# Performance work log

Measured on AMD Instinct MI355X. Metric: run time of the kernel, lower is better.

The kernel has to match this reference:

```python
import jax, jax.numpy as jnp
import numpy as np

D_MODEL = 1024
N_HEADS = 16
D_HEAD = D_MODEL // N_HEADS
HIDDEN = 4 * D_MODEL
EPS = 1e-5
ROPE_BASE = 10000.0


def layernorm(x, g, b):
    mu = jnp.mean(x, axis=-1, keepdims=True)
    var = jnp.mean((x - mu) ** 2, axis=-1, keepdims=True)
    return (x - mu) * jax.lax.rsqrt(var + EPS) * g + b


def rope(t, pos):
    # t: (B, N, D), pos: (N,) int -> rotary transform over D (half-split pairs)
    half = t.shape[-1] // 2
    inv_freq = 1.0 / (ROPE_BASE ** (jnp.arange(half, dtype=jnp.float32) / half))
    ang = pos.astype(jnp.float32)[:, None] * inv_freq  # (N, half)
    cos, sin = jnp.cos(ang), jnp.sin(ang)
    t1, t2 = t[..., :half], t[..., half:]
    return jnp.concatenate([t1 * cos - t2 * sin, t1 * sin + t2 * cos], axis=-1)


def setup_inputs() -> dict:
    key = jax.random.key(0)
    ks = jax.random.split(key, 12)
    B, N, D, H = 2, 2048, D_MODEL, HIDDEN
    s = 0.02
    return {
        "x": jax.random.normal(ks[0], (B, N, D), jnp.float32),
        "pos": jnp.arange(N, dtype=jnp.int32),
        "Wq": jax.random.normal(ks[1], (D, D), jnp.float32) * s,
        "bq": jnp.zeros((D,), jnp.float32),
        "Wk": jax.random.normal(ks[2], (D, D), jnp.float32) * s,
        "bk": jnp.zeros((D,), jnp.float32),
        "Wv": jax.random.normal(ks[3], (D, D), jnp.float32) * s,
        "bv": jnp.zeros((D,), jnp.float32),
        "Wo": jax.random.normal(ks[4], (D, D), jnp.float32) * s,
        "bo": jnp.zeros((D,), jnp.float32),
        "g1": jnp.ones((D,), jnp.float32),
        "b1": jnp.zeros((D,), jnp.float32),
        "g2": jnp.ones((D,), jnp.float32),
        "b2": jnp.zeros((D,), jnp.float32),
        "W1": jax.random.normal(ks[5], (D, H), jnp.float32) * s,
        "bm1": jnp.zeros((H,), jnp.float32),
        "W2": jax.random.normal(ks[6], (H, D), jnp.float32) * s,
        "bm2": jnp.zeros((D,), jnp.float32),
    }


def reference(x, pos, Wq, bq, Wk, bk, Wv, bv, Wo, bo, g1, b1, g2, b2, W1, bm1, W2, bm2):
    B, N, D = x.shape
    Hh, dh = N_HEADS, D_HEAD

    # --- attention sublayer (pre-norm) ---
    h = layernorm(x, g1, b1)
    q = h @ Wq + bq
    k = h @ Wk + bk
    v = h @ Wv + bv
    q = rope(q, pos)
    k = rope(k, pos)
    # split heads: (B, Hh, N, dh)
    q = q.reshape(B, N, Hh, dh).transpose(0, 2, 1, 3)
    k = k.reshape(B, N, Hh, dh).transpose(0, 2, 1, 3)
    v = v.reshape(B, N, Hh, dh).transpose(0, 2, 1, 3)
    scores = jnp.einsum("bhqd,bhkd->bhqk", q, k) / jnp.sqrt(jnp.float32(dh))
    attn = jax.nn.softmax(scores, axis=-1)
    ctx = jnp.einsum("bhqk,bhkd->bhqd", attn, v)
    ctx = ctx.transpose(0, 2, 1, 3).reshape(B, N, D)
    x = x + ctx @ Wo + bo

    # --- MLP sublayer (pre-norm, exact GELU) ---
    h = layernorm(x, g2, b2)
    h = jax.nn.gelu(h @ W1 + bm1, approximate=False)
    x = x + h @ W2 + bm2
    return x
```

## Files before the change

kernel.cpp:

```cpp
#include <hip/hip_runtime.h>

typedef __bf16 bf16x8 __attribute__((ext_vector_type(8)));
typedef __bf16 bf16x4 __attribute__((ext_vector_type(4)));
typedef float  f32x4  __attribute__((ext_vector_type(4)));

#define D_MODEL 1024
#define SEQ     2048
#define BATCH   2
#define NH      16
#define DH      64
#define HID     4096
#define ROWS    (BATCH*SEQ)

static __device__ __forceinline__ void gl_lds16(const __bf16* g, __bf16* l) {
  __builtin_amdgcn_global_load_lds(
      (const __attribute__((address_space(1))) unsigned int*)g,
      (__attribute__((address_space(3))) unsigned int*)l, 16, 0, 0);
}

__global__ __launch_bounds__(256) void ln_kernel(
    const float* __restrict__ x, const float* __restrict__ g,
    const float* __restrict__ b, __bf16* __restrict__ out)
{
  int row = blockIdx.x;
  const float* xr = x + (size_t)row * D_MODEL;
  int i0 = threadIdx.x * 4;
  f32x4 xv = *(const f32x4*)(xr + i0);
  float s  = xv[0] + xv[1] + xv[2] + xv[3];
  float ss = xv[0]*xv[0] + xv[1]*xv[1] + xv[2]*xv[2] + xv[3]*xv[3];
#pragma unroll
  for (int off = 1; off < 64; off <<= 1) {
    s  += __shfl_xor(s,  off, 64);
    ss += __shfl_xor(ss, off, 64);
  }
  __shared__ float red[8];
  int wave = threadIdx.x >> 6;
  if ((threadIdx.x & 63) == 0) { red[wave] = s; red[4 + wave] = ss; }
  __syncthreads();
  s  = red[0] + red[1] + red[2] + red[3];
  ss = red[4] + red[5] + red[6] + red[7];
  float mu  = s * (1.0f / D_MODEL);
  float var = ss * (1.0f / D_MODEL) - mu * mu;
  float inv = rsqrtf(var + 1e-5f);
  f32x4 gv = *(const f32x4*)(g + i0);
  f32x4 bv = *(const f32x4*)(b + i0);
  bf16x4 ov;
#pragma unroll
  for (int j = 0; j < 4; ++j)
    ov[j] = (__bf16)((xv[j] - mu) * inv * gv[j] + bv[j]);
  *(bf16x4*)(out + (size_t)row * D_MODEL + i0) = ov;
}

__global__ __launch_bounds__(256) void convT_kernel(
    const float* __restrict__ W, __bf16* __restrict__ Wt, int K, int N)
{
  __shared__ float T[32][33];
  int n0 = blockIdx.x * 32, k0 = blockIdx.y * 32;
  int r  = threadIdx.x >> 3;
  int c4 = (threadIdx.x & 7) * 4;
  f32x4 v = *(const f32x4*)(W + (size_t)(k0 + r) * N + n0 + c4);
#pragma unroll
  for (int i = 0; i < 4; ++i) T[r][c4 + i] = v[i];
  __syncthreads();
  bf16x4 o;
#pragma unroll
  for (int i = 0; i < 4; ++i) o[i] = (__bf16)T[c4 + i][r];
  *(bf16x4*)(Wt + (size_t)(n0 + r) * K + k0 + c4) = o;
}

__global__ void biascat_kernel(const float* __restrict__ a,
                               const float* __restrict__ b,
                               const float* __restrict__ c,
                               float* __restrict__ o)
{
  int i = blockIdx.x * 256 + threadIdx.x;
  o[i] = i < 1024 ? a[i] : (i < 2048 ? b[i - 1024] : c[i - 2048]);
}

__global__ __launch_bounds__(512, 2) void gemm256(
    const __bf16* __restrict__ A, const __bf16* __restrict__ Bt,
    const float* __restrict__ bias, const float* __restrict__ resid,
    void* __restrict__ Cv, int M, int N, int K, int act, int c_fp32)
{
  __shared__ __bf16 As[2][256 * 64];
  __shared__ __bf16 Bs[2][256 * 64];
  int tid = threadIdx.x, lane = tid & 63, wv = tid >> 6;
  int quad = lane >> 4, l16 = lane & 15;
  int wr = wv >> 2, wc = wv & 3;
  int gx = M >> 8, gy = N >> 8;
  int nwg = gx * gy;
  int xcd = blockIdx.x & 7;
  int q = nwg >> 3, r8 = nwg & 7;
  int wg = (xcd < r8 ? xcd * (q + 1) : r8 * (q + 1) + (xcd - r8) * q) + (blockIdx.x >> 3);
  int row0 = (wg % gx) << 8;
  int col0 = (wg / gx) << 8;
  int s_r  = lane >> 3;
  int s_src = ((lane & 7) ^ s_r) * 8;
  int sw = l16 & 7;
  int NT = K >> 6;
  f32x4 acc[8][4] = {};

#define G256_STAGE(kt, b)                                                     \
  {                                                                           \
    int k0_ = (kt) * 64;                                                      \
    _Pragma("unroll")                                                         \
    for (int rd = 0; rd < 4; ++rd) {                                          \
      int rrow = rd * 64 + wv * 8 + s_r;                                      \
      gl_lds16(A  + (size_t)(row0 + rrow) * K + k0_ + s_src,                  \
               &As[b][rd * 4096 + wv * 512]);                                 \
      gl_lds16(Bt + (size_t)(col0 + rrow) * K + k0_ + s_src,                  \
               &Bs[b][rd * 4096 + wv * 512]);                                 \
    }                                                                         \
  }

  G256_STAGE(0, 0);
  G256_STAGE(1, 1);

  for (int t = 0; t < NT; ++t) {
    if (t + 1 < NT) asm volatile("s_waitcnt vmcnt(8)" ::: "memory");
    else            asm volatile("s_waitcnt vmcnt(0)" ::: "memory");
    __builtin_amdgcn_s_barrier();
    const __bf16* Ab = &As[t & 1][0];
    const __bf16* Bb = &Bs[t & 1][0];
    __builtin_amdgcn_s_setprio(1);
#pragma unroll
    for (int kk = 0; kk < 2; ++kk) {
      int slot = ((kk * 4 + quad) ^ sw) * 8;
      bf16x8 bfr[4];
#pragma unroll
      for (int j = 0; j < 4; ++j)
        bfr[j] = *(const bf16x8*)(Bb + (wc * 64 + j * 16 + l16) * 64 + slot);
      bf16x8 afr[8];
#pragma unroll
      for (int i = 0; i < 8; ++i)
        afr[i] = *(const bf16x8*)(Ab + (wr * 128 + i * 16 + l16) * 64 + slot);
#pragma unroll
      for (int i = 0; i < 8; ++i)
#pragma unroll
        for (int j = 0; j < 4; ++j)
          acc[i][j] = __builtin_amdgcn_mfma_f32_16x16x32_bf16(afr[i], bfr[j], acc[i][j], 0, 0, 0);
    }
    __builtin_amdgcn_s_setprio(0);
    __builtin_amdgcn_s_barrier();
    if (t + 2 < NT) G256_STAGE(t + 2, t & 1);
  }

#pragma unroll
  for (int i = 0; i < 8; ++i) {
    int grow = row0 + wr * 128 + i * 16 + quad * 4;
#pragma unroll
    for (int j = 0; j < 4; ++j) {
      int gcol = col0 + wc * 64 + j * 16 + l16;
      float bsv = bias[gcol];
#pragma unroll
      for (int r = 0; r < 4; ++r) {
        size_t off = (size_t)(grow + r) * N + gcol;
        float v = acc[i][j][r] + bsv;
        if (act) v = 0.5f * v * (1.0f + erff(v * 0.70710678118654752f));
        if (resid) v += resid[off];
        if (c_fp32) ((float*)Cv)[off] = v;
        else        ((__bf16*)Cv)[off] = (__bf16)v;
      }
    }
  }
}

__global__ __launch_bounds__(256) void gemm128(
    const __bf16* __restrict__ A, const __bf16* __restrict__ Bt,
    const float* __restrict__ bias, const float* __restrict__ resid,
    void* __restrict__ Cv, int M, int N, int K, int act, int c_fp32)
{
  __shared__ __bf16 As[128 * 64];
  __shared__ __bf16 Bs[128 * 64];
  int tid = threadIdx.x, lane = tid & 63, wv = tid >> 6;
  int quad = lane >> 4, l16 = lane & 15;
  int wr = wv >> 1, wc = wv & 1;
  int gx = M >> 7, gy = N >> 7;
  int blk = blockIdx.x;
  int xcd = blk & 7, t = blk >> 3;
  int row0 = (t % gx) * 128;
  int col0 = (xcd * (gy >> 3) + t / gx) * 128;
  int s_r8 = lane >> 3;
  int s_c8 = lane & 7;
  int s_src = (s_c8 ^ s_r8) * 8;
  int sw = l16 & 7;
  f32x4 acc[4][4] = {};

  for (int k0 = 0; k0 < K; k0 += 64) {
#pragma unroll
    for (int p = 0; p < 4; ++p) {
      int r = p * 32 + wv * 8 + s_r8;
      gl_lds16(A  + (size_t)(row0 + r) * K + k0 + s_src, As + p * 2048 + wv * 512);
      gl_lds16(Bt + (size_t)(col0 + r) * K + k0 + s_src, Bs + p * 2048 + wv * 512);
    }
    __syncthreads();
#pragma unroll
    for (int kk = 0; kk < 2; ++kk) {
      int slot = ((kk * 4 + quad) ^ sw) * 8;
      bf16x8 af[4], bf[4];
#pragma unroll
      for (int i = 0; i < 4; ++i) {
        af[i] = *(const bf16x8*)(As + (wr * 64 + i * 16 + l16) * 64 + slot);
        bf[i] = *(const bf16x8*)(Bs + (wc * 64 + i * 16 + l16) * 64 + slot);
      }
#pragma unroll
      for (int i = 0; i < 4; ++i)
#pragma unroll
        for (int j = 0; j < 4; ++j)
          acc[i][j] = __builtin_amdgcn_mfma_f32_16x16x32_bf16(af[i], bf[j], acc[i][j], 0, 0, 0);
    }
    __syncthreads();
  }
#pragma unroll
  for (int i = 0; i < 4; ++i) {
    int grow = row0 + wr * 64 + i * 16 + quad * 4;
#pragma unroll
    for (int j = 0; j < 4; ++j) {
      int gcol = col0 + wc * 64 + j * 16 + l16;
      float bsv = bias[gcol];
#pragma unroll
      for (int r = 0; r < 4; ++r) {
        size_t off = (size_t)(grow + r) * N + gcol;
        float v = acc[i][j][r] + bsv;
        if (act) v = 0.5f * v * (1.0f + erff(v * 0.70710678118654752f));
        if (resid) v += resid[off];
        if (c_fp32) ((float*)Cv)[off] = v;
        else        ((__bf16*)Cv)[off] = (__bf16)v;
      }
    }
  }
}

__global__ __launch_bounds__(256) void gemm64x128(
    const __bf16* __restrict__ A, const __bf16* __restrict__ Bt,
    const float* __restrict__ bias, const float* __restrict__ resid,
    void* __restrict__ Cv, int M, int N, int K, int act, int c_fp32)
{
  __shared__ __bf16 As[2][64 * 64];
  __shared__ __bf16 Bs[2][128 * 64];
  int tid = threadIdx.x, lane = tid & 63, wv = tid >> 6;
  int quad = lane >> 4, l16 = lane & 15;
  int wr = wv >> 1, wc = wv & 1;
  int gx = M >> 6, gy = N >> 7;
  int blk = blockIdx.x;
  int xcd = blk & 7, t = blk >> 3;
  int row0 = (t % gx) * 64;
  int col0 = (xcd * (gy >> 3) + t / gx) * 128;
  int s_r8 = lane >> 3;
  int s_c8 = lane & 7;
  int s_src = (s_c8 ^ s_r8) * 8;
  int sw = l16 & 7;
  int NT = K >> 6;
  f32x4 acc[2][4] = {};

#define G64_STAGE(kt, b)                                                      \
  {                                                                           \
    int k0_ = (kt) * 64;                                                      \
    _Pragma("unroll")                                                         \
    for (int p = 0; p < 4; ++p) {                                             \
      int r = p * 32 + wv * 8 + s_r8;                                         \
      if (p < 2)                                                              \
        gl_lds16(A + (size_t)(row0 + r) * K + k0_ + s_src,                    \
                 &As[b][p * 2048 + wv * 512]);                                \
      gl_lds16(Bt + (size_t)(col0 + r) * K + k0_ + s_src,                     \
               &Bs[b][p * 2048 + wv * 512]);                                  \
    }                                                                         \
  }

  G64_STAGE(0, 0);
  G64_STAGE(1, 1);

  for (int tt = 0; tt < NT; ++tt) {
    if (tt + 1 < NT) asm volatile("s_waitcnt vmcnt(6)" ::: "memory");
    else             asm volatile("s_waitcnt vmcnt(0)" ::: "memory");
    __builtin_amdgcn_s_barrier();
    const __bf16* Ab = &As[tt & 1][0];
    const __bf16* Bb = &Bs[tt & 1][0];
    __builtin_amdgcn_s_setprio(1);
#pragma unroll
    for (int kk = 0; kk < 2; ++kk) {
      int slot = ((kk * 4 + quad) ^ sw) * 8;
      bf16x8 af[2], bf[4];
#pragma unroll
      for (int i = 0; i < 2; ++i)
        af[i] = *(const bf16x8*)(Ab + (wr * 32 + i * 16 + l16) * 64 + slot);
#pragma unroll
      for (int j = 0; j < 4; ++j)
        bf[j] = *(const bf16x8*)(Bb + (wc * 64 + j * 16 + l16) * 64 + slot);
#pragma unroll
      for (int i = 0; i < 2; ++i)
#pragma unroll
        for (int j = 0; j < 4; ++j)
          acc[i][j] = __builtin_amdgcn_mfma_f32_16x16x32_bf16(af[i], bf[j], acc[i][j], 0, 0, 0);
    }
    __builtin_amdgcn_s_setprio(0);
    __builtin_amdgcn_s_barrier();
    if (tt + 2 < NT) G64_STAGE(tt + 2, tt & 1);
  }

#pragma unroll
  for (int i = 0; i < 2; ++i) {
    int grow = row0 + wr * 32 + i * 16 + quad * 4;
#pragma unroll
    for (int j = 0; j < 4; ++j) {
      int gcol = col0 + wc * 64 + j * 16 + l16;
      float bsv = bias[gcol];
#pragma unroll
      for (int r = 0; r < 4; ++r) {
        size_t off = (size_t)(grow + r) * N + gcol;
        float v = acc[i][j][r] + bsv;
        if (act) v = 0.5f * v * (1.0f + erff(v * 0.70710678118654752f));
        if (resid) v += resid[off];
        if (c_fp32) ((float*)Cv)[off] = v;
        else        ((__bf16*)Cv)[off] = (__bf16)v;
      }
    }
  }
}

__global__ __launch_bounds__(256) void rope_repack(
    const __bf16* __restrict__ qkv, const int* __restrict__ pos,
    __bf16* __restrict__ Qh, __bf16* __restrict__ Kh)
{
  int row = blockIdx.x;
  int b = row >> 11, n = row & (SEQ - 1);
  float p = (float)pos[n];
  const __bf16* qr = qkv + (size_t)row * 3072;
  const float QS = 0.125f * 1.44269504088896f;
#pragma unroll
  for (int t = 0; t < 2; ++t) {
    int i = threadIdx.x + t * 256;
    float fr  = expf(-9.210340371976184f * ((float)i * (1.0f / 512.0f)));
    float ang = p * fr;
    float sn, c;
    sincosf(ang, &sn, &c);
    float q1 = (float)qr[i],        q2 = (float)qr[512 + i];
    float k1 = (float)qr[1024 + i], k2 = (float)qr[1536 + i];
    int h1 = i >> 6, d1 = i & 63;
    int h2 = (i + 512) >> 6;
    size_t o1 = ((size_t)(b * NH + h1) * SEQ + n) * DH + d1;
    size_t o2 = ((size_t)(b * NH + h2) * SEQ + n) * DH + d1;
    Qh[o1] = (__bf16)((q1 * c - q2 * sn) * QS);
    Qh[o2] = (__bf16)((q1 * sn + q2 * c) * QS);
    Kh[o1] = (__bf16)(k1 * c - k2 * sn);
    Kh[o2] = (__bf16)(k1 * sn + k2 * c);
  }
}

__global__ __launch_bounds__(256) void vtrans_kernel(
    const __bf16* __restrict__ Vsrc, int vstride, __bf16* __restrict__ Vt,
    int blocked)
{
  __shared__ __bf16 T[64][72];
  int bh = blockIdx.x;
  int kb = blockIdx.y * 64;
  int b = bh >> 4, h = bh & 15;
  int tid = threadIdx.x;
#pragma unroll
  for (int t = 0; t < 2; ++t) {
    int u = tid + t * 256;
    int r = u >> 3, seg = (u & 7) * 8;
    bf16x8 v = *(const bf16x8*)(Vsrc + (size_t)(b * SEQ + kb + r) * vstride + h * DH + seg);
    *(bf16x8*)(&T[r][seg]) = v;
  }
  __syncthreads();
#pragma unroll
  for (int t = 0; t < 2; ++t) {
    int u = tid + t * 256;
    int d = u >> 3, ks = (u & 7) * 8;
    bf16x8 o;
#pragma unroll
    for (int i = 0; i < 8; ++i) o[i] = T[ks + i][d];
    if (blocked) {
      int key = kb + ks;
      *(bf16x8*)(Vt + (((size_t)bh * (SEQ / 128) + (key >> 7)) * DH + d) * 128 + (key & 127)) = o;
    } else {
      *(bf16x8*)(Vt + ((size_t)bh * DH + d) * SEQ + kb + ks) = o;
    }
  }
}

#define KS 136
__global__ __launch_bounds__(512) void attn_split(
    const __bf16* __restrict__ Qh, const __bf16* __restrict__ Kh,
    const __bf16* __restrict__ Vt, __bf16* __restrict__ pacc,
    float* __restrict__ pml)
{
  __shared__ __bf16 Ks[128 * 64];
  __shared__ __bf16 Vs[64 * 128];
  __shared__ __bf16 Pl[8][16 * KS];
  int tid = threadIdx.x, lane = tid & 63, wave = tid >> 6;
  int quad = lane >> 4, l16 = lane & 15;
  int blk = blockIdx.x;
  int split = blk >> 9;
  int rr = blk & 511;
  int bh  = ((rr & 7) << 2) | ((rr >> 3) & 3);
  int q128 = rr >> 5;
  int q0 = q128 * 128 + wave * 16;
  const __bf16* qbase = Qh + (size_t)bh * SEQ * DH;
  const __bf16* kbase = Kh + (size_t)bh * SEQ * DH;
  const __bf16* vbase = Vt + (size_t)bh * SEQ * DH;
  const __bf16* qp = qbase + (size_t)(q0 + l16) * DH + quad * 8;
  bf16x8 qf0 = *(const bf16x8*)(qp);
  bf16x8 qf1 = *(const bf16x8*)(qp + 32);
  float lrow[4] = {0.f, 0.f, 0.f, 0.f};
  f32x4 acc[4] = {};
  __bf16* pw = &Pl[wave][0];
  int s_kr = lane >> 3;
  int s_k8 = lane & 7;
  int s_vd = lane >> 4;
  int s_vs = lane & 15;
  int sw8  = l16 & 7;

  int kb0 = split * (SEQ / 2);
  for (int it = 0; it < (SEQ / 2) / 128; ++it) {
    int kb = kb0 + it * 128;
    const __bf16* kt = kbase + (size_t)kb * DH;
    const __bf16* vt = vbase + (size_t)(kb >> 7) * (DH * 128);
    __syncthreads();
#pragma unroll
    for (int p = 0; p < 2; ++p) {
      int key0 = p * 64 + wave * 8;
      int swz  = (key0 >> 3) & 7;
      gl_lds16(kt + (key0 + s_kr) * DH + ((s_k8 ^ swz) * 8), Ks + p * 4096 + wave * 512);
      int d = p * 32 + wave * 4 + s_vd;
      gl_lds16(vt + d * 128 + ((s_vs ^ (d & 15)) * 8), Vs + p * 4096 + wave * 512);
    }
    __syncthreads();
    f32x4 s[8];
#pragma unroll
    for (int j = 0; j < 8; ++j) {
      const __bf16* kr = Ks + (l16 * 8 + j) * 64;
      bf16x8 kf0 = *(const bf16x8*)(kr + (quad ^ sw8) * 8);
      bf16x8 kf1 = *(const bf16x8*)(kr + ((quad ^ sw8) ^ 4) * 8);
      f32x4 z = {};
      z = __builtin_amdgcn_mfma_f32_16x16x32_bf16(qf0, kf0, z, 0, 0, 0);
      s[j] = __builtin_amdgcn_mfma_f32_16x16x32_bf16(qf1, kf1, z, 0, 0, 0);
    }
#pragma unroll
    for (int r = 0; r < 4; ++r) {
      bf16x8 pv;
      float rs = 0.f;
#pragma unroll
      for (int j = 0; j < 8; ++j) {
        float pj = exp2f(s[j][r]);
        rs += pj;
        pv[j] = (__bf16)pj;
      }
      lrow[r] += rs;
      *(bf16x8*)(pw + (quad * 4 + r) * KS + l16 * 8) = pv;
    }
#pragma unroll
    for (int kk = 0; kk < 4; ++kk) {
      bf16x8 pf = *(const bf16x8*)(pw + l16 * KS + kk * 32 + quad * 8);
#pragma unroll
      for (int j = 0; j < 4; ++j) {
        int d = j * 16 + l16;
        bf16x8 vf = *(const bf16x8*)(Vs + d * 128 + (((kk * 4 + quad) ^ (d & 15)) * 8));
        acc[j] = __builtin_amdgcn_mfma_f32_16x16x32_bf16(pf, vf, acc[j], 0, 0, 0);
      }
    }
  }
#pragma unroll
  for (int r = 0; r < 4; ++r)
#pragma unroll
    for (int off = 1; off < 16; off <<= 1) lrow[r] += __shfl_xor(lrow[r], off, 64);
#pragma unroll
  for (int r = 0; r < 4; ++r) {
    int brow = wave * 16 + quad * 4 + r;
#pragma unroll
    for (int j = 0; j < 4; ++j)
      pacc[((size_t)blk * 128 + brow) * 64 + j * 16 + l16] = (__bf16)acc[j][r];
    if (l16 == 0) {
      pml[(size_t)blk * 256 + brow]       = 0.f;
      pml[(size_t)blk * 256 + 128 + brow] = lrow[r];
    }
  }
}

__global__ __launch_bounds__(256) void attn_combine(
    const __bf16* __restrict__ pacc, const float* __restrict__ pml,
    __bf16* __restrict__ ctx)
{
  int bq = blockIdx.x;
  int q64 = bq & 31, bh = bq >> 5;
  int b = bh >> 4, h = bh & 15;
  int q128 = q64 >> 1, half = q64 & 1;
  int tid = threadIdx.x;
  int r = tid >> 2;
  int c = (tid & 3) * 16;
  int brow = half * 64 + r;
  int blk0 = q128 * 32 + (bh & 3) * 8 + (bh >> 2);
  int blk1 = blk0 + 512;
  float m0 = pml[(size_t)blk0 * 256 + brow], l0 = pml[(size_t)blk0 * 256 + 128 + brow];
  float m1 = pml[(size_t)blk1 * 256 + brow], l1 = pml[(size_t)blk1 * 256 + 128 + brow];
  float m = fmaxf(m0, m1);
  float w0 = __expf(m0 - m), w1 = __expf(m1 - m);
  float inv = 1.0f / (w0 * l0 + w1 * l1);
  size_t r0 = ((size_t)blk0 * 128 + brow) * 64 + c;
  size_t r1 = ((size_t)blk1 * 128 + brow) * 64 + c;
  size_t ob = ((size_t)(b * SEQ) + q64 * 64 + r) * D_MODEL + h * DH + c;
#pragma unroll
  for (int g = 0; g < 2; ++g) {
    bf16x8 a0 = *(const bf16x8*)(pacc + r0 + g * 8);
    bf16x8 a1 = *(const bf16x8*)(pacc + r1 + g * 8);
    bf16x8 o;
#pragma unroll
    for (int i = 0; i < 8; ++i)
      o[i] = (__bf16)((w0 * (float)a0[i] + w1 * (float)a1[i]) * inv);
    *(bf16x8*)(ctx + ob + g * 8) = o;
  }
}

__global__ __launch_bounds__(256) void rope_inplace(
    __bf16* __restrict__ ql, __bf16* __restrict__ kl,
    const int* __restrict__ pos, int stride)
{
  int row = blockIdx.x;
  int n = row & (SEQ - 1);
  float p = (float)pos[n];
  const size_t rbase = (size_t)row * stride;
#pragma unroll
  for (int t = 0; t < 2; ++t) {
    int i = threadIdx.x + t * 256;
    float fr  = expf(-9.210340371976184f * ((float)i * (1.0f / 512.0f)));
    float ang = p * fr;
    float sn, c;
    sincosf(ang, &sn, &c);
    float q1 = (float)ql[rbase + i], q2 = (float)ql[rbase + 512 + i];
    float k1 = (float)kl[rbase + i], k2 = (float)kl[rbase + 512 + i];
    ql[rbase + i]       = (__bf16)(q1 * c - q2 * sn);
    ql[rbase + 512 + i] = (__bf16)(q1 * sn + q2 * c);
    kl[rbase + i]       = (__bf16)(k1 * c - k2 * sn);
    kl[rbase + 512 + i] = (__bf16)(k1 * sn + k2 * c);
  }
}

__global__ __launch_bounds__(256) void attn_kernel(
    const __bf16* __restrict__ Q, const __bf16* __restrict__ K,
    const __bf16* __restrict__ Vt, __bf16* __restrict__ ctx, int qkstride)
{
  __shared__ __bf16 Pl[4][16 * KS];
  int tid = threadIdx.x, lane = tid & 63, wave = tid >> 6;
  int quad = lane >> 4, l16 = lane & 15;
  int blk = blockIdx.x;
  int q64 = blk & 31;
  int bh  = blk >> 5;
  int b = bh >> 4, h = bh & 15;
  int q0 = q64 * 64 + wave * 16;
  const __bf16* qbase = Q + (size_t)b * SEQ * qkstride + h * DH;
  const __bf16* kbase = K + (size_t)b * SEQ * qkstride + h * DH;
  const __bf16* vbase = Vt + (size_t)bh * DH * SEQ;
  const __bf16* qp = qbase + (size_t)(q0 + l16) * qkstride + quad * 8;
  bf16x8 qf0 = *(const bf16x8*)(qp);
  bf16x8 qf1 = *(const bf16x8*)(qp + 32);
  float mrow[4] = {-1e30f, -1e30f, -1e30f, -1e30f};
  float lrow[4] = {0.f, 0.f, 0.f, 0.f};
  f32x4 acc[4] = {};
  __bf16* pw = &Pl[wave][0];

  for (int kb = 0; kb < SEQ; kb += 128) {
    f32x4 s[8];
#pragma unroll
    for (int j = 0; j < 8; ++j) {
      const __bf16* kp = kbase + (size_t)(kb + l16 * 8 + j) * qkstride + quad * 8;
      bf16x8 kf0 = *(const bf16x8*)(kp);
      bf16x8 kf1 = *(const bf16x8*)(kp + 32);
      f32x4 z = {};
      z = __builtin_amdgcn_mfma_f32_16x16x32_bf16(qf0, kf0, z, 0, 0, 0);
      z = __builtin_amdgcn_mfma_f32_16x16x32_bf16(qf1, kf1, z, 0, 0, 0);
#pragma unroll
      for (int r = 0; r < 4; ++r) s[j][r] = z[r] * 0.125f;
    }
#pragma unroll
    for (int r = 0; r < 4; ++r) {
      float mx = s[0][r];
#pragma unroll
      for (int j = 1; j < 8; ++j) mx = fmaxf(mx, s[j][r]);
#pragma unroll
      for (int off = 1; off < 16; off <<= 1) mx = fmaxf(mx, __shfl_xor(mx, off, 64));
      float mn = fmaxf(mrow[r], mx);
      float al = __expf(mrow[r] - mn);
      float p[8], rs = 0.f;
#pragma unroll
      for (int j = 0; j < 8; ++j) { p[j] = __expf(s[j][r] - mn); rs += p[j]; }
#pragma unroll
      for (int off = 1; off < 16; off <<= 1) rs += __shfl_xor(rs, off, 64);
      lrow[r] = lrow[r] * al + rs;
      mrow[r] = mn;
#pragma unroll
      for (int j = 0; j < 4; ++j) acc[j][r] *= al;
      bf16x8 pv;
#pragma unroll
      for (int j = 0; j < 8; ++j) pv[j] = (__bf16)p[j];
      *(bf16x8*)(pw + (quad * 4 + r) * KS + l16 * 8) = pv;
    }
#pragma unroll
    for (int kk = 0; kk < 4; ++kk) {
      bf16x8 pf = *(const bf16x8*)(pw + l16 * KS + kk * 32 + quad * 8);
#pragma unroll
      for (int j = 0; j < 4; ++j) {
        bf16x8 vf = *(const bf16x8*)(vbase + (size_t)(j * 16 + l16) * SEQ + kb + kk * 32 + quad * 8);
        acc[j] = __builtin_amdgcn_mfma_f32_16x16x32_bf16(pf, vf, acc[j], 0, 0, 0);
      }
    }
  }
#pragma unroll
  for (int r = 0; r < 4; ++r) {
    int row = q0 + quad * 4 + r;
    float inv = 1.0f / lrow[r];
    size_t obase = ((size_t)(b * SEQ) + row) * D_MODEL + h * DH;
#pragma unroll
    for (int j = 0; j < 4; ++j)
      ctx[obase + j * 16 + l16] = (__bf16)(acc[j][r] * inv);
  }
}

extern "C" void kernel_launch(void* const* d_in, const int* in_sizes, int n_in,
                              void* d_out, int out_size, void* d_ws, size_t ws_size,
                              hipStream_t stream)
{
  const float* x   = (const float*)d_in[0];
  const int*   pos = (const int*)  d_in[1];
  const float* Wq  = (const float*)d_in[2];
  const float* bq  = (const float*)d_in[3];
  const float* Wk  = (const float*)d_in[4];
  const float* bk  = (const float*)d_in[5];
  const float* Wv  = (const float*)d_in[6];
  const float* bv  = (const float*)d_in[7];
  const float* Wo  = (const float*)d_in[8];
  const float* bo  = (const float*)d_in[9];
  const float* g1  = (const float*)d_in[10];
  const float* b1  = (const float*)d_in[11];
  const float* g2  = (const float*)d_in[12];
  const float* b2  = (const float*)d_in[13];
  const float* W1  = (const float*)d_in[14];
  const float* bm1 = (const float*)d_in[15];
  const float* W2  = (const float*)d_in[16];
  const float* bm2 = (const float*)d_in[17];
  float* out = (float*)d_out;

  const size_t MB = 1024 * 1024;
  char* w = (char*)d_ws;
  dim3 blk(256);
  dim3 blk512(512);
  dim3 gConvD(D_MODEL / 32, D_MODEL / 32);
  dim3 gConv1(HID / 32, D_MODEL / 32);
  dim3 gConv2(D_MODEL / 32, HID / 32);
  dim3 gVt(BATCH * NH, SEQ / 64);

  if (ws_size >= (size_t)96 * MB) {
    __bf16* hln   = (__bf16*)(w + 0 * MB);
    float*  x1    = (float*) (w + 8 * MB);
    __bf16* qkv   = (__bf16*)(w + 24 * MB);
    __bf16* pacc  = (__bf16*)(w + 24 * MB);
    float*  pml   = (float*) (w + 41 * MB);
    __bf16* hmlp  = (__bf16*)(w + 24 * MB);
    __bf16* Qh    = (__bf16*)(w + 48 * MB);
    __bf16* ctx   = (__bf16*)(w + 48 * MB);
    __bf16* Kh    = (__bf16*)(w + 56 * MB);
    __bf16* W2T   = (__bf16*)(w + 56 * MB);
    __bf16* Vt    = (__bf16*)(w + 64 * MB);
    __bf16* W1T   = (__bf16*)(w + 64 * MB);
    __bf16* WqkvT = (__bf16*)(w + 72 * MB);
    __bf16* WoT   = (__bf16*)(w + 78 * MB);
    float*  bqkv  = (float*) (w + 80 * MB);

    convT_kernel<<<gConvD, blk, 0, stream>>>(Wq, WqkvT,               D_MODEL, D_MODEL);
    convT_kernel<<<gConvD, blk, 0, stream>>>(Wk, WqkvT + 1024 * 1024, D_MODEL, D_MODEL);
    convT_kernel<<<gConvD, blk, 0, stream>>>(Wv, WqkvT + 2048 * 1024, D_MODEL, D_MODEL);
    convT_kernel<<<gConvD, blk, 0, stream>>>(Wo, WoT, D_MODEL, D_MODEL);
    biascat_kernel<<<12, blk, 0, stream>>>(bq, bk, bv, bqkv);
    ln_kernel<<<ROWS, blk, 0, stream>>>(x, g1, b1, hln);
    gemm256<<<(ROWS / 256) * (3072 / 256), blk512, 0, stream>>>(hln, WqkvT, bqkv, nullptr, qkv, ROWS, 3072, D_MODEL, 0, 0);
    rope_repack<<<ROWS, blk, 0, stream>>>(qkv, pos, Qh, Kh);
    vtrans_kernel<<<gVt, blk, 0, stream>>>(qkv + 2048, 3072, Vt, 1);
    attn_split<<<BATCH * NH * (SEQ / 128) * 2, blk512, 0, stream>>>(Qh, Kh, Vt, pacc, pml);
    attn_combine<<<BATCH * NH * (SEQ / 64), blk, 0, stream>>>(pacc, pml, ctx);
    convT_kernel<<<gConv1, blk, 0, stream>>>(W1, W1T, D_MODEL, HID);
    convT_kernel<<<gConv2, blk, 0, stream>>>(W2, W2T, HID, D_MODEL);
    gemm64x128<<<(ROWS / 64) * (D_MODEL / 128), blk, 0, stream>>>(ctx, WoT, bo, x, x1, ROWS, D_MODEL, D_MODEL, 0, 1);
    ln_kernel<<<ROWS, blk, 0, stream>>>(x1, g2, b2, hln);
    gemm256<<<(ROWS / 256) * (HID / 256), blk512, 0, stream>>>(hln, W1T, bm1, nullptr, hmlp, ROWS, HID, D_MODEL, 1, 0);
    gemm64x128<<<(ROWS / 64) * (D_MODEL / 128), blk, 0, stream>>>(hmlp, W2T, bm2, x1, out, ROWS, D_MODEL, HID, 0, 1);
  } else {
    __bf16* hln  = (__bf16*)(w + 0 * MB);
    __bf16* vlin = (__bf16*)(w + 8 * MB);
    __bf16* WqT  = (__bf16*)(w + 16 * MB);
    __bf16* WkT  = (__bf16*)(w + 18 * MB);
    __bf16* WvT  = (__bf16*)(w + 20 * MB);
    __bf16* ctx  = (__bf16*)(w + 16 * MB);
    __bf16* WoT  = (__bf16*)(w + 8 * MB);
    __bf16* W1T  = (__bf16*)(w + 8 * MB);
    __bf16* W2T  = (__bf16*)(w + 16 * MB);
    __bf16* Vt   = (__bf16*)(w + 24 * MB);
    __bf16* hmlp = (__bf16*)(w + 24 * MB);
    __bf16* qlin = (__bf16*)d_out;
    __bf16* klin = (__bf16*)d_out + (size_t)ROWS * D_MODEL;
    float*  x1   = (float*)d_out;

    convT_kernel<<<gConvD, blk, 0, stream>>>(Wq, WqT, D_MODEL, D_MODEL);
    convT_kernel<<<gConvD, blk, 0, stream>>>(Wk, WkT, D_MODEL, D_MODEL);
    convT_kernel<<<gConvD, blk, 0, stream>>>(Wv, WvT, D_MODEL, D_MODEL);
    ln_kernel<<<ROWS, blk, 0, stream>>>(x, g1, b1, hln);
    int nLin = (ROWS / 64) * (D_MODEL / 128);
    gemm64x128<<<nLin, blk, 0, stream>>>(hln, WqT, bq, nullptr, qlin, ROWS, D_MODEL, D_MODEL, 0, 0);
    gemm64x128<<<nLin, blk, 0, stream>>>(hln, WkT, bk, nullptr, klin, ROWS, D_MODEL, D_MODEL, 0, 0);
    gemm64x128<<<nLin, blk, 0, stream>>>(hln, WvT, bv, nullptr, vlin, ROWS, D_MODEL, D_MODEL, 0, 0);
    rope_inplace<<<ROWS, blk, 0, stream>>>(qlin, klin, pos, D_MODEL);
    vtrans_kernel<<<gVt, blk, 0, stream>>>(vlin, D_MODEL, Vt, 0);
    attn_kernel<<<BATCH * NH * (SEQ / 64), blk, 0, stream>>>(qlin, klin, Vt, ctx, D_MODEL);
    convT_kernel<<<gConvD, blk, 0, stream>>>(Wo, WoT, D_MODEL, D_MODEL);
    gemm64x128<<<nLin, blk, 0, stream>>>(ctx, WoT, bo, x, x1, ROWS, D_MODEL, D_MODEL, 0, 1);
    ln_kernel<<<ROWS, blk, 0, stream>>>(x1, g2, b2, hln);
    convT_kernel<<<gConv1, blk, 0, stream>>>(W1, W1T, D_MODEL, HID);
    convT_kernel<<<gConv2, blk, 0, stream>>>(W2, W2T, HID, D_MODEL);
    const int CH = 1024;
    for (int c = 0; c < ROWS / CH; ++c) {
      const __bf16* a1 = hln + (size_t)c * CH * D_MODEL;
      gemm128<<<(CH / 128) * (HID / 128), blk, 0, stream>>>(a1, W1T, bm1, nullptr, hmlp, CH, HID, D_MODEL, 1, 0);
      gemm64x128<<<(CH / 64) * (D_MODEL / 128), blk, 0, stream>>>(hmlp, W2T, bm2, x1 + (size_t)c * CH * D_MODEL,
                                          out + (size_t)c * CH * D_MODEL, CH, D_MODEL, HID, 0, 1);
    }
  }
}
```

Baseline: 448.0 us.

## Halve attention block to 4 waves, each handling two 16-row query tiles

The split attention kernel now runs 256 threads per block instead of 512, and each wave processes two 16-row query tiles against the shared K/V tiles in LDS. K and V fragments are reused across more query rows per wave, and the LDS for P staging shrinks. The exp2f call is also replaced with the hardware exp2 builtin. In exchange each wave holds twice the accumulators and Q fragments, which raises register pressure and leaves fewer waves to hide load latency.

```diff
diff --git a/kernel.cpp b/kernel.cpp
--- a/kernel.cpp
+++ b/kernel.cpp
@@ -381,14 +381,14 @@
 }
 
 #define KS 136
-__global__ __launch_bounds__(512) void attn_split(
+__global__ __launch_bounds__(256) void attn_split(
     const __bf16* __restrict__ Qh, const __bf16* __restrict__ Kh,
     const __bf16* __restrict__ Vt, __bf16* __restrict__ pacc,
     float* __restrict__ pml)
 {
   __shared__ __bf16 Ks[128 * 64];
   __shared__ __bf16 Vs[64 * 128];
-  __shared__ __bf16 Pl[8][16 * KS];
+  __shared__ __bf16 Pl[4][16 * KS];
   int tid = threadIdx.x, lane = tid & 63, wave = tid >> 6;
   int quad = lane >> 4, l16 = lane & 15;
   int blk = blockIdx.x;
@@ -396,15 +396,18 @@
   int rr = blk & 511;
   int bh  = ((rr & 7) << 2) | ((rr >> 3) & 3);
   int q128 = rr >> 5;
-  int q0 = q128 * 128 + wave * 16;
   const __bf16* qbase = Qh + (size_t)bh * SEQ * DH;
   const __bf16* kbase = Kh + (size_t)bh * SEQ * DH;
   const __bf16* vbase = Vt + (size_t)bh * SEQ * DH;
-  const __bf16* qp = qbase + (size_t)(q0 + l16) * DH + quad * 8;
-  bf16x8 qf0 = *(const bf16x8*)(qp);
-  bf16x8 qf1 = *(const bf16x8*)(qp + 32);
-  float lrow[4] = {0.f, 0.f, 0.f, 0.f};
-  f32x4 acc[4] = {};
+  bf16x8 qf0[2], qf1[2];
+#pragma unroll
+  for (int h = 0; h < 2; ++h) {
+    const __bf16* qp = qbase + (size_t)(q128 * 128 + h * 64 + wave * 16 + l16) * DH + quad * 8;
+    qf0[h] = *(const bf16x8*)(qp);
+    qf1[h] = *(const bf16x8*)(qp + 32);
+  }
+  float lrow[2][4] = {};
+  f32x4 acc[2][4] = {};
   __bf16* pw = &Pl[wave][0];
   int s_kr = lane >> 3;
   int s_k8 = lane & 7;
@@ -419,63 +422,70 @@
     const __bf16* vt = vbase + (size_t)(kb >> 7) * (DH * 128);
     __syncthreads();
 #pragma unroll
-    for (int p = 0; p < 2; ++p) {
-      int key0 = p * 64 + wave * 8;
+    for (int p = 0; p < 4; ++p) {
+      int key0 = p * 32 + wave * 8;
       int swz  = (key0 >> 3) & 7;
-      gl_lds16(kt + (key0 + s_kr) * DH + ((s_k8 ^ swz) * 8), Ks + p * 4096 + wave * 512);
-      int d = p * 32 + wave * 4 + s_vd;
-      gl_lds16(vt + d * 128 + ((s_vs ^ (d & 15)) * 8), Vs + p * 4096 + wave * 512);
+      gl_lds16(kt + (key0 + s_kr) * DH + ((s_k8 ^ swz) * 8), Ks + p * 2048 + wave * 512);
+      int d = p * 16 + wave * 4 + s_vd;
+      gl_lds16(vt + d * 128 + ((s_vs ^ (d & 15)) * 8), Vs + p * 2048 + wave * 512);
     }
     __syncthreads();
-    f32x4 s[8];
-#pragma unroll
-    for (int j = 0; j < 8; ++j) {
-      const __bf16* kr = Ks + (l16 * 8 + j) * 64;
-      bf16x8 kf0 = *(const bf16x8*)(kr + (quad ^ sw8) * 8);
-      bf16x8 kf1 = *(const bf16x8*)(kr + ((quad ^ sw8) ^ 4) * 8);
-      f32x4 z = {};
-      z = __builtin_amdgcn_mfma_f32_16x16x32_bf16(qf0, kf0, z, 0, 0, 0);
-      s[j] = __builtin_amdgcn_mfma_f32_16x16x32_bf16(qf1, kf1, z, 0, 0, 0);
-    }
+#pragma unroll
+    for (int h = 0; h < 2; ++h) {
+      f32x4 s[8];
+#pragma unroll
+      for (int j = 0; j < 8; ++j) {
+        const __bf16* kr = Ks + (l16 * 8 + j) * 64;
+        bf16x8 kf0 = *(const bf16x8*)(kr + (quad ^ sw8) * 8);
+        bf16x8 kf1 = *(const bf16x8*)(kr + ((quad ^ sw8) ^ 4) * 8);
+        f32x4 z = {};
+        z = __builtin_amdgcn_mfma_f32_16x16x32_bf16(qf0[h], kf0, z, 0, 0, 0);
+        s[j] = __builtin_amdgcn_mfma_f32_16x16x32_bf16(qf1[h], kf1, z, 0, 0, 0);
+      }
+#pragma unroll
+      for (int r = 0; r < 4; ++r) {
+        bf16x8 pv;
+        float rs = 0.f;
+#pragma unroll
+        for (int j = 0; j < 8; ++j) {
+          float pj = __builtin_amdgcn_exp2f(s[j][r]);
+          rs += pj;
+          pv[j] = (__bf16)pj;
+        }
+        lrow[h][r] += rs;
+        *(bf16x8*)(pw + (quad * 4 + r) * KS + l16 * 8) = pv;
+      }
+#pragma unroll
+      for (int kk = 0; kk < 4; ++kk) {
+        bf16x8 pf = *(const bf16x8*)(pw + l16 * KS + kk * 32 + quad * 8);
+#pragma unroll
+        for (int j = 0; j < 4; ++j) {
+          int d = j * 16 + l16;
+          bf16x8 vf = *(const bf16x8*)(Vs + d * 128 + (((kk * 4 + quad) ^ (d & 15)) * 8));
+          acc[h][j] = __builtin_amdgcn_mfma_f32_16x16x32_bf16(pf, vf, acc[h][j], 0, 0, 0);
+        }
+      }
+    }
+  }
+#pragma unroll
+  for (int h = 0; h < 2; ++h)
+#pragma unroll
+    for (int r = 0; r < 4; ++r)
+#pragma unroll
+      for (int off = 1; off < 16; off <<= 1) lrow[h][r] += __shfl_xor(lrow[h][r], off, 64);
+#pragma unroll
+  for (int h = 0; h < 2; ++h)
 #pragma unroll
     for (int r = 0; r < 4; ++r) {
-      bf16x8 pv;
-      float rs = 0.f;
-#pragma unroll
-      for (int j = 0; j < 8; ++j) {
-        float pj = exp2f(s[j][r]);
-        rs += pj;
-        pv[j] = (__bf16)pj;
-      }
-      lrow[r] += rs;
-      *(bf16x8*)(pw + (quad * 4 + r) * KS + l16 * 8) = pv;
-    }
-#pragma unroll
-    for (int kk = 0; kk < 4; ++kk) {
-      bf16x8 pf = *(const bf16x8*)(pw + l16 * KS + kk * 32 + quad * 8);
-#pragma unroll
-      for (int j = 0; j < 4; ++j) {
-        int d = j * 16 + l16;
-        bf16x8 vf = *(const bf16x8*)(Vs + d * 128 + (((kk * 4 + quad) ^ (d & 15)) * 8));
-        acc[j] = __builtin_amdgcn_mfma_f32_16x16x32_bf16(pf, vf, acc[j], 0, 0, 0);
-      }
-    }
-  }
-#pragma unroll
-  for (int r = 0; r < 4; ++r)
-#pragma unroll
-    for (int off = 1; off < 16; off <<= 1) lrow[r] += __shfl_xor(lrow[r], off, 64);
-#pragma unroll
-  for (int r = 0; r < 4; ++r) {
-    int brow = wave * 16 + quad * 4 + r;
-#pragma unroll
-    for (int j = 0; j < 4; ++j)
-      pacc[((size_t)blk * 128 + brow) * 64 + j * 16 + l16] = (__bf16)acc[j][r];
-    if (l16 == 0) {
-      pml[(size_t)blk * 256 + brow]       = 0.f;
-      pml[(size_t)blk * 256 + 128 + brow] = lrow[r];
-    }
-  }
+      int brow = h * 64 + wave * 16 + quad * 4 + r;
+#pragma unroll
+      for (int j = 0; j < 4; ++j)
+        pacc[((size_t)blk * 128 + brow) * 64 + j * 16 + l16] = (__bf16)acc[h][j][r];
+      if (l16 == 0) {
+        pml[(size_t)blk * 256 + brow]       = 0.f;
+        pml[(size_t)blk * 256 + 128 + brow] = lrow[h][r];
+      }
+    }
 }
 
 __global__ __launch_bounds__(256) void attn_combine(
@@ -675,7 +685,7 @@
     gemm256<<<(ROWS / 256) * (3072 / 256), blk512, 0, stream>>>(hln, WqkvT, bqkv, nullptr, qkv, ROWS, 3072, D_MODEL, 0, 0);
     rope_repack<<<ROWS, blk, 0, stream>>>(qkv, pos, Qh, Kh);
     vtrans_kernel<<<gVt, blk, 0, stream>>>(qkv + 2048, 3072, Vt, 1);
-    attn_split<<<BATCH * NH * (SEQ / 128) * 2, blk512, 0, stream>>>(Qh, Kh, Vt, pacc, pml);
+    attn_split<<<BATCH * NH * (SEQ / 128) * 2, blk, 0, stream>>>(Qh, Kh, Vt, pacc, pml);
     attn_combine<<<BATCH * NH * (SEQ / 64), blk, 0, stream>>>(pacc, pml, ctx);
     convT_kernel<<<gConv1, blk, 0, stream>>>(W1, W1T, D_MODEL, HID);
     convT_kernel<<<gConv2, blk, 0, stream>>>(W2, W2T, HID, D_MODEL);
```

Measured after the change: 423.5 us. 1.06x faster.
